# Kernel optimization log

Measured on AMD Instinct MI355X. Metric: run time of the kernel, lower is better.

The kernel has to match this reference:

```python
import jax, jax.numpy as jnp
import numpy as np

N_EMBD = 1024
N_HEAD = 16
BASE_SCALE = 0.03125  # config.base_scale
ATTN_ALPHA_INIT = 0.05
MLP_ALPHA_INIT = 0.05
SQK_INIT = 1.0
SUV_INIT = 1.0


def justnorm(x):
    return x / jnp.linalg.norm(x, axis=-1, keepdims=True)


def normalized_linear(x, W):
    # F.normalize(weight, p=2, dim=0): unit-norm columns of W [out, in] across the out dim
    Wn = W / jnp.linalg.norm(W, axis=0, keepdims=True)
    return x @ Wn.T


def setup_inputs() -> dict:
    key = jax.random.key(0)
    ks = jax.random.split(key, 8)
    C = N_EMBD
    s = 1.0 / np.sqrt(C)
    inp = {
        "h": jax.random.normal(ks[0], (8, 1024, C), dtype=jnp.float32),
        "Wq": jax.random.normal(ks[1], (C, C), dtype=jnp.float32) * s,
        "Wk": jax.random.normal(ks[2], (C, C), dtype=jnp.float32) * s,
        "Wv": jax.random.normal(ks[3], (C, C), dtype=jnp.float32) * s,
        "Wo": jax.random.normal(ks[4], (C, C), dtype=jnp.float32) * s,
        "Wfc": jax.random.normal(ks[5], (8 * C, C), dtype=jnp.float32) * s,
        "Wproj": jax.random.normal(ks[6], (C, 4 * C), dtype=jnp.float32) * (1.0 / np.sqrt(4 * C)),
        "sqk": jnp.full((C,), SQK_INIT * BASE_SCALE, dtype=jnp.float32),
        "suv": jnp.full((8 * C,), SUV_INIT * 1.0, dtype=jnp.float32),
        "attn_alpha": jnp.full((C,), BASE_SCALE, dtype=jnp.float32),
        "mlp_alpha": jnp.full((C,), BASE_SCALE, dtype=jnp.float32),
    }
    return inp


def reference(h, Wq, Wk, Wv, Wo, Wfc, Wproj, sqk, suv, attn_alpha, mlp_alpha):
    B, T, C = h.shape
    H, D = N_HEAD, C // N_HEAD

    # ---- attention ----
    q = normalized_linear(h, Wq).reshape(B, T, H, D).transpose(0, 2, 1, 3)  # bhtd
    k = normalized_linear(h, Wk).reshape(B, T, H, D).transpose(0, 2, 1, 3)
    v = normalized_linear(h, Wv).reshape(B, T, H, D).transpose(0, 2, 1, 3)

    sqk_s = (sqk * (SQK_INIT / BASE_SCALE)).reshape(1, H, 1, D)  # per-(head, head_dim) scale
    q = sqk_s * justnorm(q)
    k = sqk_s * justnorm(k)

    softmax_scale = float(D) ** 0.5  # nGPT uses sqrt(head_dim)
    att = jax.nn.softmax(jnp.einsum("bhqd,bhkd->bhqk", q, k) * softmax_scale, axis=-1)
    y = jnp.einsum("bhqk,bhkd->bhqd", att, v)
    y = y.transpose(0, 2, 1, 3).reshape(B, T, C)
    h_att = normalized_linear(y, Wo)

    lr = jnp.abs(attn_alpha * (ATTN_ALPHA_INIT / BASE_SCALE))
    A = justnorm(h)
    Bn = justnorm(h_att)
    h = justnorm(A + lr * (Bn - A))

    # ---- SwiGLU MLP ----
    uv = h @ Wfc.T  # [B,T,8C]
    suv_s = suv * (SUV_INIT / 1.0 * (C ** 0.5))
    uv = suv_s * uv
    u, vg = jnp.split(uv, 2, axis=-1)
    x_mlp = u * jax.nn.silu(vg)
    h_mlp = x_mlp @ Wproj.T

    lr = jnp.abs(mlp_alpha * (MLP_ALPHA_INIT / BASE_SCALE))
    A = justnorm(h)
    Bn = justnorm(h_mlp)
    h = justnorm(A + lr * (Bn - A))
    return h
```

## Files before the change

kernel.cpp:

```cpp
#include <hip/hip_runtime.h>

typedef __attribute__((ext_vector_type(8))) short s8v;
typedef __attribute__((ext_vector_type(4))) short s4v;
typedef __attribute__((ext_vector_type(4))) float f4v;

#define MFMA __builtin_amdgcn_mfma_f32_16x16x32_bf16

__device__ __forceinline__ float b2f(unsigned short b) {
  union { unsigned u; float f; } x; x.u = ((unsigned)b) << 16; return x.f;
}
__device__ __forceinline__ unsigned short f2b(float f) {
  union { float f; unsigned u; } x; x.f = f;
  unsigned r = x.u + 0x7fffu + ((x.u >> 16) & 1u);
  return (unsigned short)(r >> 16);
}
__device__ __forceinline__ void gl_lds16(const void* g, void* l) {
  __builtin_amdgcn_global_load_lds(
      (const __attribute__((address_space(1))) unsigned int*)g,
      (__attribute__((address_space(3))) unsigned int*)l, 16, 0, 0);
}

__global__ void colsq4(const float* __restrict__ Wq, const float* __restrict__ Wk,
                       const float* __restrict__ Wv, const float* __restrict__ Wo,
                       float* __restrict__ cs) {
  const int z = blockIdx.z;
  const float* W = (z == 0) ? Wq : (z == 1) ? Wk : (z == 2) ? Wv : Wo;
  int j = blockIdx.x * 256 + threadIdx.x;
  const float* p = W + (long)(blockIdx.y * 64) * 1024 + j;
  float s = 0.f;
#pragma unroll 4
  for (int n = 0; n < 64; ++n) { float v = p[(long)n * 1024]; s += v * v; }
  atomicAdd(&cs[z * 1024 + j], s);
}

__global__ void convw4(const float* __restrict__ Wq, const float* __restrict__ Wk,
                       const float* __restrict__ Wv, const float* __restrict__ Wo,
                       const float* __restrict__ cs, unsigned short* __restrict__ dst) {
  const int y = blockIdx.y;
  const float* src = (y == 0) ? Wq : (y == 1) ? Wk : (y == 2) ? Wv : Wo;
  long idx = ((long)blockIdx.x * 256 + threadIdx.x) << 2;
  float4 v = *(const float4*)(src + idx);
  const float* c = cs + y * 1024 + (int)(idx & 1023);
  s4v o;
  o[0] = (short)f2b(v.x * rsqrtf(c[0]));
  o[1] = (short)f2b(v.y * rsqrtf(c[1]));
  o[2] = (short)f2b(v.z * rsqrtf(c[2]));
  o[3] = (short)f2b(v.w * rsqrtf(c[3]));
  *(s4v*)(dst + (long)y * 1048576 + idx) = o;
}

__global__ void cast3(const float* __restrict__ Wfc, const float* __restrict__ Wpj,
                      const float* __restrict__ h, unsigned short* __restrict__ Wfc_b,
                      unsigned short* __restrict__ Wpj_b, unsigned short* __restrict__ h_b) {
  int bid = blockIdx.x;
  const float* src; unsigned short* dst;
  if (bid < 8192) { src = Wfc; dst = Wfc_b; }
  else if (bid < 12288) { src = Wpj; dst = Wpj_b; bid -= 8192; }
  else { src = h; dst = h_b; bid -= 12288; }
  long idx = ((long)bid * 256 + threadIdx.x) << 2;
  float4 v = *(const float4*)(src + idx);
  s4v o;
  o[0] = (short)f2b(v.x); o[1] = (short)f2b(v.y);
  o[2] = (short)f2b(v.z); o[3] = (short)f2b(v.w);
  *(s4v*)(dst + idx) = o;
}

__global__ __launch_bounds__(256) void gemm_bt(
    const unsigned short* __restrict__ A, const unsigned short* __restrict__ B,
    unsigned short* __restrict__ Cout, int K, int ldc) {
  __shared__ unsigned short smem[32768];
  const int tid = threadIdx.x, lane = tid & 63, w = tid >> 6;
  const int quad = lane >> 4, lq = lane & 15;
  const int wy = w >> 1, wx = w & 1;
  const int m0 = blockIdx.y << 7, n0 = blockIdx.x << 7;

  const int trow = tid >> 2;
  const int cb = ((tid & 3) ^ ((tid >> 3) & 3)) << 3;
  const unsigned short* Ag0 = A + (long)(m0 + trow) * K + cb;
  const unsigned short* Ag1 = A + (long)(m0 + 64 + trow) * K + cb;
  const unsigned short* Bg0 = B + (long)(n0 + trow) * K + cb;
  const unsigned short* Bg1 = B + (long)(n0 + 64 + trow) * K + cb;
  unsigned short* l0 = smem + (tid << 3);

  const int swz = ((lq >> 1) & 3) << 4;
  const int aoff = (wy * 64 + lq) * 64 + ((quad << 4) ^ swz);
  const int boff = 8192 + (wx * 64 + lq) * 64 + ((quad << 4) ^ swz);

  f4v acc[4][4];
  f4v zero = {0.f, 0.f, 0.f, 0.f};
#pragma unroll
  for (int i = 0; i < 4; ++i)
#pragma unroll
    for (int j = 0; j < 4; ++j) acc[i][j] = zero;

  auto stage = [&](int T) {
    const int bo = (T & 3) << 13;
    const int col = T << 5;
    gl_lds16(Ag0 + col, l0 + bo);
    gl_lds16(Ag1 + col, l0 + bo + 2048);
    gl_lds16(Bg0 + col, l0 + bo + 4096);
    gl_lds16(Bg1 + col, l0 + bo + 6144);
  };
  const char* sb = (const char*)smem;
  auto compute = [&](int kt) {
    const int bo = (kt & 3) << 14;
    s8v a[4], b[4];
#pragma unroll
    for (int i = 0; i < 4; ++i) a[i] = *(const s8v*)(sb + bo + aoff + i * 1024);
#pragma unroll
    for (int j = 0; j < 4; ++j) b[j] = *(const s8v*)(sb + bo + boff + j * 1024);
    __builtin_amdgcn_s_setprio(1);
#pragma unroll
    for (int i = 0; i < 4; ++i)
#pragma unroll
      for (int j = 0; j < 4; ++j)
        acc[i][j] = MFMA(a[i], b[j], acc[i][j], 0, 0, 0);
    __builtin_amdgcn_s_setprio(0);
  };

  const int nt = K >> 5;
  stage(0); stage(1); stage(2);
  for (int kt = 0; kt < nt - 2; ++kt) {
    asm volatile("s_waitcnt vmcnt(8)" ::: "memory");
    __builtin_amdgcn_s_barrier();
    asm volatile("" ::: "memory");
    if (kt < nt - 3) stage(kt + 3);
    compute(kt);
  }
  asm volatile("s_waitcnt vmcnt(4)" ::: "memory");
  __builtin_amdgcn_s_barrier();
  asm volatile("" ::: "memory");
  compute(nt - 2);
  asm volatile("s_waitcnt vmcnt(0)" ::: "memory");
  __builtin_amdgcn_s_barrier();
  asm volatile("" ::: "memory");
  compute(nt - 1);

  __syncthreads();
#pragma unroll
  for (int i = 0; i < 4; ++i)
#pragma unroll
    for (int j = 0; j < 4; ++j)
#pragma unroll
      for (int r = 0; r < 4; ++r) {
        int row = wy * 64 + i * 16 + quad * 4 + r;
        int col = wx * 64 + j * 16 + lq;
        smem[row * 136 + col] = f2b(acc[i][j][r]);
      }
  __syncthreads();
#pragma unroll
  for (int it = 0; it < 8; ++it) {
    int row = it * 16 + (tid >> 4);
    int col = (tid & 15) << 3;
    s8v v = *(const s8v*)(smem + row * 136 + col);
    *(s8v*)(Cout + (long)(m0 + row) * ldc + n0 + col) = v;
  }
}

__global__ __launch_bounds__(256) void gemm_qkv(
    const unsigned short* __restrict__ A, const unsigned short* __restrict__ B,
    unsigned short* __restrict__ Cout, unsigned short* __restrict__ Vt,
    const float* __restrict__ sqk) {
  __shared__ unsigned short smem[32768];
  const int tid = threadIdx.x, lane = tid & 63, w = tid >> 6;
  const int quad = lane >> 4, lq = lane & 15;
  const int wy = w >> 1, wx = w & 1;
  const int m0 = blockIdx.y << 7, n0 = blockIdx.x << 7;
  const int K = 1024;

  const int trow = tid >> 2;
  const int cb = ((tid & 3) ^ ((tid >> 3) & 3)) << 3;
  const unsigned short* Ag0 = A + (long)(m0 + trow) * K + cb;
  const unsigned short* Ag1 = A + (long)(m0 + 64 + trow) * K + cb;
  const unsigned short* Bg0 = B + (long)(n0 + trow) * K + cb;
  const unsigned short* Bg1 = B + (long)(n0 + 64 + trow) * K + cb;
  unsigned short* l0 = smem + (tid << 3);

  const int swz = ((lq >> 1) & 3) << 4;
  const int aoff = (wy * 64 + lq) * 64 + ((quad << 4) ^ swz);
  const int boff = 8192 + (wx * 64 + lq) * 64 + ((quad << 4) ^ swz);

  f4v acc[4][4];
  f4v zero = {0.f, 0.f, 0.f, 0.f};
#pragma unroll
  for (int i = 0; i < 4; ++i)
#pragma unroll
    for (int j = 0; j < 4; ++j) acc[i][j] = zero;

  auto stage = [&](int T) {
    const int bo = (T & 3) << 13;
    const int col = T << 5;
    gl_lds16(Ag0 + col, l0 + bo);
    gl_lds16(Ag1 + col, l0 + bo + 2048);
    gl_lds16(Bg0 + col, l0 + bo + 4096);
    gl_lds16(Bg1 + col, l0 + bo + 6144);
  };
  const char* sb = (const char*)smem;
  auto compute = [&](int kt) {
    const int bo = (kt & 3) << 14;
    s8v a[4], b[4];
#pragma unroll
    for (int i = 0; i < 4; ++i) a[i] = *(const s8v*)(sb + bo + aoff + i * 1024);
#pragma unroll
    for (int j = 0; j < 4; ++j) b[j] = *(const s8v*)(sb + bo + boff + j * 1024);
    __builtin_amdgcn_s_setprio(1);
#pragma unroll
    for (int i = 0; i < 4; ++i)
#pragma unroll
      for (int j = 0; j < 4; ++j)
        acc[i][j] = MFMA(a[i], b[j], acc[i][j], 0, 0, 0);
    __builtin_amdgcn_s_setprio(0);
  };

  stage(0); stage(1); stage(2);
  for (int kt = 0; kt < 30; ++kt) {
    asm volatile("s_waitcnt vmcnt(8)" ::: "memory");
    __builtin_amdgcn_s_barrier();
    asm volatile("" ::: "memory");
    if (kt < 29) stage(kt + 3);
    compute(kt);
  }
  asm volatile("s_waitcnt vmcnt(4)" ::: "memory");
  __builtin_amdgcn_s_barrier();
  asm volatile("" ::: "memory");
  compute(30);
  asm volatile("s_waitcnt vmcnt(0)" ::: "memory");
  __builtin_amdgcn_s_barrier();
  asm volatile("" ::: "memory");
  compute(31);

  if (n0 < 2048) {
    float sc[4];
#pragma unroll
    for (int j = 0; j < 4; ++j)
      sc[j] = sqk[(n0 + wx * 64 + j * 16 + lq) & 1023] * 32.f;
#pragma unroll
    for (int i = 0; i < 4; ++i)
#pragma unroll
      for (int r = 0; r < 4; ++r) {
        float ss = 0.f;
#pragma unroll
        for (int j = 0; j < 4; ++j) ss += acc[i][j][r] * acc[i][j][r];
        ss += __shfl_xor(ss, 1, 64); ss += __shfl_xor(ss, 2, 64);
        ss += __shfl_xor(ss, 4, 64); ss += __shfl_xor(ss, 8, 64);
        float rn = rsqrtf(ss);
#pragma unroll
        for (int j = 0; j < 4; ++j) acc[i][j][r] *= rn * sc[j];
      }
    __syncthreads();
#pragma unroll
    for (int i = 0; i < 4; ++i)
#pragma unroll
      for (int j = 0; j < 4; ++j)
#pragma unroll
        for (int r = 0; r < 4; ++r) {
          int row = wy * 64 + i * 16 + quad * 4 + r;
          int col = wx * 64 + j * 16 + lq;
          smem[row * 136 + col] = f2b(acc[i][j][r]);
        }
    __syncthreads();
#pragma unroll
    for (int it = 0; it < 8; ++it) {
      int row = it * 16 + (tid >> 4);
      int col = (tid & 15) << 3;
      s8v v = *(const s8v*)(smem + row * 136 + col);
      *(s8v*)(Cout + (long)(m0 + row) * 3072 + n0 + col) = v;
    }
  } else {
    __syncthreads();
#pragma unroll
    for (int i = 0; i < 4; ++i)
#pragma unroll
      for (int j = 0; j < 4; ++j) {
        int col = wx * 64 + j * 16 + lq;
        int rowb = wy * 64 + i * 16 + quad * 4;
        s4v pk;
#pragma unroll
        for (int r = 0; r < 4; ++r) pk[r] = (short)f2b(acc[i][j][r]);
        *(s4v*)(smem + col * 136 + rowb) = pk;
      }
    __syncthreads();
    {
      const int c = tid >> 1, half = tid & 1;
      const int f = (n0 - 2048) + c;
      const int bh = ((m0 >> 10) << 4) + (f >> 6);
      const int d = f & 63;
      unsigned short* dst = Vt + (long)(bh * 64 + d) * 1024 + (m0 & 1023) + half * 64;
      const unsigned short* src = smem + c * 136 + half * 64;
#pragma unroll
      for (int s = 0; s < 8; ++s)
        *(s8v*)(dst + s * 8) = *(const s8v*)(src + s * 8);
    }
  }
}

__global__ __launch_bounds__(512, 2) void gemm_fc(
    const unsigned short* __restrict__ A, const unsigned short* __restrict__ B,
    unsigned short* __restrict__ X, const float* __restrict__ suv) {
  __shared__ unsigned short smem[65536];
  const int tid = threadIdx.x, lane = tid & 63, w = tid >> 6;
  const int quad = lane >> 4, lq = lane & 15;
  const int wy = w >> 2, wx = w & 3;
  const int bid = blockIdx.x;
  const int xr = bid & 7, xq = bid >> 3;
  const int m0 = ((xr << 2) | (xq & 3)) << 8;
  const int n0 = (xq >> 2) << 7;

  const int trow = tid >> 3;
  const int scol = ((tid & 7) ^ (trow & 7)) << 3;
  const unsigned short* pA = A + (long)(m0 + trow) * 1024 + scol;
  const unsigned short* pB = B + (long)(n0 + trow) * 1024 + scol;
  unsigned short* ldst = smem + tid * 8;

  auto stA = [&](int tile, int half) {
    const int base = (tile & 1) * 32768 + half * 8192;
    const unsigned short* src = pA + (long)half * 131072 + (tile << 6);
    gl_lds16(src, ldst + base);
    gl_lds16(src + 65536, ldst + base + 4096);
  };
  auto stB = [&](int tile, int vh) {
    const int base = (tile & 1) * 32768 + 16384 + vh * 8192;
    const unsigned short* src = pB + (long)vh * 4194304 + (tile << 6);
    gl_lds16(src, ldst + base);
    gl_lds16(src + 65536, ldst + base + 4096);
  };

  const int rsw = (lq & 7) << 4;
  const int c0 = (quad * 16) ^ rsw;
  const int c1 = (64 + quad * 16) ^ rsw;
  const int aro = wy * 16384 + lq * 128;
  const int uro = 32768 + (wx * 32 + lq) * 128;
  const int vro = 49152 + (wx * 32 + lq) * 128;
  const char* sb = (const char*)smem;

  f4v aU[8][2], aV[8][2];
  f4v zero = {0.f, 0.f, 0.f, 0.f};
#pragma unroll
  for (int m = 0; m < 8; ++m)
#pragma unroll
    for (int j = 0; j < 2; ++j) { aU[m][j] = zero; aV[m][j] = zero; }

  s8v av[4][2], uf[2][2], vg[2][2];

  auto tile_phases = [&](int t, int bufB) {
#pragma unroll
    for (int m = 0; m < 4; ++m) {
      av[m][0] = *(const s8v*)(sb + bufB + aro + m * 2048 + c0);
      av[m][1] = *(const s8v*)(sb + bufB + aro + m * 2048 + c1);
    }
#pragma unroll
    for (int j = 0; j < 2; ++j) {
      uf[j][0] = *(const s8v*)(sb + bufB + uro + j * 2048 + c0);
      uf[j][1] = *(const s8v*)(sb + bufB + uro + j * 2048 + c1);
    }
    if (t < 15) stA(t + 1, 1);
    __builtin_amdgcn_s_barrier();
    asm volatile("" ::: "memory");
    __builtin_amdgcn_s_setprio(1);
#pragma unroll
    for (int m = 0; m < 4; ++m)
#pragma unroll
      for (int j = 0; j < 2; ++j) {
        aU[m][j] = MFMA(av[m][0], uf[j][0], aU[m][j], 0, 0, 0);
        aU[m][j] = MFMA(av[m][1], uf[j][1], aU[m][j], 0, 0, 0);
      }
    __builtin_amdgcn_s_setprio(0);
    asm volatile("" ::: "memory");
    __builtin_amdgcn_s_barrier();
    asm volatile("" ::: "memory");
#pragma unroll
    for (int j = 0; j < 2; ++j) {
      vg[j][0] = *(const s8v*)(sb + bufB + vro + j * 2048 + c0);
      vg[j][1] = *(const s8v*)(sb + bufB + vro + j * 2048 + c1);
    }
    if (t < 14) stB(t + 2, 0);
    __builtin_amdgcn_s_barrier();
    asm volatile("" ::: "memory");
    __builtin_amdgcn_s_setprio(1);
#pragma unroll
    for (int m = 0; m < 4; ++m)
#pragma unroll
      for (int j = 0; j < 2; ++j) {
        aV[m][j] = MFMA(av[m][0], vg[j][0], aV[m][j], 0, 0, 0);
        aV[m][j] = MFMA(av[m][1], vg[j][1], aV[m][j], 0, 0, 0);
      }
    __builtin_amdgcn_s_setprio(0);
    asm volatile("" ::: "memory");
    __builtin_amdgcn_s_barrier();
    asm volatile("" ::: "memory");
#pragma unroll
    for (int m = 0; m < 4; ++m) {
      av[m][0] = *(const s8v*)(sb + bufB + aro + (m + 4) * 2048 + c0);
      av[m][1] = *(const s8v*)(sb + bufB + aro + (m + 4) * 2048 + c1);
    }
    if (t < 14) stB(t + 2, 1);
    __builtin_amdgcn_s_barrier();
    asm volatile("" ::: "memory");
    __builtin_amdgcn_s_setprio(1);
#pragma unroll
    for (int m = 0; m < 4; ++m)
#pragma unroll
      for (int j = 0; j < 2; ++j) {
        aU[m + 4][j] = MFMA(av[m][0], uf[j][0], aU[m + 4][j], 0, 0, 0);
        aU[m + 4][j] = MFMA(av[m][1], uf[j][1], aU[m + 4][j], 0, 0, 0);
      }
    __builtin_amdgcn_s_setprio(0);
    asm volatile("" ::: "memory");
    __builtin_amdgcn_s_barrier();
    asm volatile("" ::: "memory");
    if (t < 14) stA(t + 2, 0);
    __builtin_amdgcn_s_barrier();
    asm volatile("" ::: "memory");
    __builtin_amdgcn_s_setprio(1);
#pragma unroll
    for (int m = 0; m < 4; ++m)
#pragma unroll
      for (int j = 0; j < 2; ++j) {
        aV[m + 4][j] = MFMA(av[m][0], vg[j][0], aV[m + 4][j], 0, 0, 0);
        aV[m + 4][j] = MFMA(av[m][1], vg[j][1], aV[m + 4][j], 0, 0, 0);
      }
    __builtin_amdgcn_s_setprio(0);
    if (t < 14) { asm volatile("s_waitcnt vmcnt(6)" ::: "memory"); }
    else if (t == 14) { asm volatile("s_waitcnt vmcnt(0)" ::: "memory"); }
    asm volatile("" ::: "memory");
    __builtin_amdgcn_s_barrier();
    asm volatile("" ::: "memory");
  };

  stB(0, 0); stB(0, 1); stA(0, 0); stA(0, 1);
  stB(1, 0); stB(1, 1); stA(1, 0);
  asm volatile("s_waitcnt vmcnt(6)" ::: "memory");
  __builtin_amdgcn_s_barrier();
  asm volatile("" ::: "memory");

  for (int tt = 0; tt < 8; ++tt) {
    tile_phases(tt * 2, 0);
    tile_phases(tt * 2 + 1, 65536);
  }

  float su[2], sv[2];
#pragma unroll
  for (int j = 0; j < 2; ++j) {
    su[j] = suv[n0 + wx * 32 + j * 16 + lq] * 32.f;
    sv[j] = suv[4096 + n0 + wx * 32 + j * 16 + lq] * 32.f;
  }
  __syncthreads();
#pragma unroll
  for (int m = 0; m < 8; ++m)
#pragma unroll
    for (int j = 0; j < 2; ++j)
#pragma unroll
      for (int r = 0; r < 4; ++r) {
        int row = wy * 128 + m * 16 + quad * 4 + r;
        int col = wx * 32 + j * 16 + lq;
        float uu = aU[m][j][r] * su[j];
        float vv = aV[m][j][r] * sv[j];
        float sig = 1.f / (1.f + __builtin_amdgcn_exp2f(vv * -1.44269504f));
        smem[row * 132 + col] = f2b(uu * vv * sig);
      }
  __syncthreads();
  {
    const int row = tid >> 1, half = tid & 1;
    unsigned short* dst = X + (long)(m0 + row) * 4096 + n0 + half * 64;
    const unsigned short* srcr = smem + row * 132 + half * 64;
#pragma unroll
    for (int s = 0; s < 8; ++s)
      *(s8v*)(dst + s * 8) = *(const s8v*)(srcr + s * 8);
  }
}

__global__ __launch_bounds__(256) void attn(const unsigned short* __restrict__ qkv,
                                            const unsigned short* __restrict__ Vt,
                                            unsigned short* __restrict__ Y) {
  __shared__ unsigned short smem[33792];
  unsigned short* Klds = smem;
  unsigned short* Vlds = smem + 8192;
  unsigned short* Plds = smem + 16384;
  const int tid = threadIdx.x, lane = tid & 63, w = tid >> 6;
  const int quad = lane >> 4, lq = lane & 15;
  const int bh = blockIdx.x, b = bh >> 4, h = bh & 15;
  const int qt = blockIdx.y;
  const int e0 = tid << 3;
  const int c_lo = e0 >> 10, row_s = (e0 & 1023) >> 3;
  const int vc_lo = e0 >> 9, vd = (e0 & 511) >> 3;

  s8v qf[2][2];
#pragma unroll
  for (int i = 0; i < 2; ++i)
#pragma unroll
    for (int ks = 0; ks < 2; ++ks) {
      int row = qt * 128 + w * 32 + i * 16 + lq;
      qf[i][ks] = *(const s8v*)(qkv + (long)(b * 1024 + row) * 3072 + h * 64 + ks * 32 + quad * 8);
    }

  f4v o[2][4];
  float lp[2][4];
  f4v zero = {0.f, 0.f, 0.f, 0.f};
#pragma unroll
  for (int i = 0; i < 2; ++i) {
#pragma unroll
    for (int nf = 0; nf < 4; ++nf) o[i][nf] = zero;
#pragma unroll
    for (int r = 0; r < 4; ++r) lp[i][r] = 0.f;
  }

  const unsigned short* Kg = qkv + (long)(b * 1024 + row_s) * 3072 + 1024 + h * 64 + (c_lo << 3);
  const unsigned short* Vg = Vt + (long)(bh * 64 + vd) * 1024 + (vc_lo << 3);
  unsigned short* Pw = Plds + w * 4352;

  for (int kt0 = 0; kt0 < 1024; kt0 += 128) {
    __syncthreads();
#pragma unroll
    for (int it = 0; it < 4; ++it) {
      gl_lds16(Kg + (long)kt0 * 3072 + it * 16, Klds + it * 2048 + e0);
      gl_lds16(Vg + kt0 + it * 32, Vlds + it * 2048 + e0);
    }
    __syncthreads();
    f4v s[2][8];
#pragma unroll
    for (int i = 0; i < 2; ++i)
#pragma unroll
      for (int j = 0; j < 8; ++j) s[i][j] = zero;
#pragma unroll
    for (int ks = 0; ks < 2; ++ks)
#pragma unroll
      for (int j = 0; j < 8; ++j) {
        s8v kf = *(const s8v*)(Klds + (ks * 4 + quad) * 1024 + (j * 16 + lq) * 8);
        s[0][j] = MFMA(qf[0][ks], kf, s[0][j], 0, 0, 0);
        s[1][j] = MFMA(qf[1][ks], kf, s[1][j], 0, 0, 0);
      }
#pragma unroll
    for (int i = 0; i < 2; ++i)
#pragma unroll
      for (int j = 0; j < 8; ++j)
#pragma unroll
        for (int r = 0; r < 4; ++r) {
          float p = __builtin_amdgcn_exp2f(s[i][j][r] * 11.5415603f - 11.5415603f);
          lp[i][r] += p;
          Pw[(i * 16 + quad * 4 + r) * 136 + j * 16 + lq] = f2b(p);
        }
    s8v pf[2][4];
#pragma unroll
    for (int i = 0; i < 2; ++i)
#pragma unroll
      for (int ks = 0; ks < 4; ++ks)
        pf[i][ks] = *(const s8v*)(Pw + (i * 16 + lq) * 136 + ks * 32 + quad * 8);
#pragma unroll
    for (int nf = 0; nf < 4; ++nf)
#pragma unroll
      for (int ks = 0; ks < 4; ++ks) {
        s8v vf = *(const s8v*)(Vlds + (ks * 4 + quad) * 512 + (nf * 16 + lq) * 8);
        o[0][nf] = MFMA(pf[0][ks], vf, o[0][nf], 0, 0, 0);
        o[1][nf] = MFMA(pf[1][ks], vf, o[1][nf], 0, 0, 0);
      }
  }
#pragma unroll
  for (int i = 0; i < 2; ++i)
#pragma unroll
    for (int r = 0; r < 4; ++r) {
      float v = lp[i][r];
      v += __shfl_xor(v, 1, 64); v += __shfl_xor(v, 2, 64);
      v += __shfl_xor(v, 4, 64); v += __shfl_xor(v, 8, 64);
      lp[i][r] = 1.f / v;
    }
#pragma unroll
  for (int i = 0; i < 2; ++i)
#pragma unroll
    for (int nf = 0; nf < 4; ++nf)
#pragma unroll
      for (int r = 0; r < 4; ++r) {
        int row = qt * 128 + w * 32 + i * 16 + quad * 4 + r;
        Y[(long)(b * 1024 + row) * 1024 + h * 64 + nf * 16 + lq] = f2b(o[i][nf][r] * lp[i][r]);
      }
}

__global__ __launch_bounds__(256) void residual(
    const float* __restrict__ hin, const unsigned short* __restrict__ hbr,
    const float* __restrict__ alpha, float* __restrict__ outf,
    unsigned short* __restrict__ outb) {
  __shared__ float red[8];
  const int tid = threadIdx.x, lane = tid & 63, w = tid >> 6;
  const long base = (long)blockIdx.x * 1024;
  float hv[4], bvv[4];
  float s1 = 0.f, s2 = 0.f;
#pragma unroll
  for (int k = 0; k < 4; ++k) {
    int c = k * 256 + tid;
    hv[k] = hin[base + c];
    bvv[k] = b2f(hbr[base + c]);
    s1 += hv[k] * hv[k]; s2 += bvv[k] * bvv[k];
  }
#pragma unroll
  for (int m = 1; m < 64; m <<= 1) { s1 += __shfl_xor(s1, m, 64); s2 += __shfl_xor(s2, m, 64); }
  if (lane == 0) { red[w] = s1; red[4 + w] = s2; }
  __syncthreads();
  s1 = red[0] + red[1] + red[2] + red[3];
  s2 = red[4] + red[5] + red[6] + red[7];
  float rn1 = rsqrtf(s1), rn2 = rsqrtf(s2);
  float z[4], s3 = 0.f;
#pragma unroll
  for (int k = 0; k < 4; ++k) {
    int c = k * 256 + tid;
    float a = hv[k] * rn1;
    float lr = fabsf(alpha[c]) * 1.6f;
    float zz = a + lr * (bvv[k] * rn2 - a);
    z[k] = zz; s3 += zz * zz;
  }
#pragma unroll
  for (int m = 1; m < 64; m <<= 1) s3 += __shfl_xor(s3, m, 64);
  __syncthreads();
  if (lane == 0) red[w] = s3;
  __syncthreads();
  s3 = red[0] + red[1] + red[2] + red[3];
  float rn3 = rsqrtf(s3);
#pragma unroll
  for (int k = 0; k < 4; ++k) {
    int c = k * 256 + tid;
    float ov = z[k] * rn3;
    if (outf) outf[base + c] = ov;
    if (outb) outb[base + c] = f2b(ov);
  }
}

extern "C" void kernel_launch(void* const* d_in, const int* in_sizes, int n_in,
                              void* d_out, int out_size, void* d_ws, size_t ws_size,
                              hipStream_t stream) {
  const float* h   = (const float*)d_in[0];
  const float* Wq  = (const float*)d_in[1];
  const float* Wk  = (const float*)d_in[2];
  const float* Wv  = (const float*)d_in[3];
  const float* Wo  = (const float*)d_in[4];
  const float* Wfc = (const float*)d_in[5];
  const float* Wpj = (const float*)d_in[6];
  const float* sqk = (const float*)d_in[7];
  const float* suv = (const float*)d_in[8];
  const float* aat = (const float*)d_in[9];
  const float* aml = (const float*)d_in[10];
  float* out = (float*)d_out;

  char* ws = (char*)d_ws;
  size_t off = 0;
  auto alloc = [&](size_t n) { char* p = ws + off; off += (n + 255) & ~(size_t)255; return p; };
  float* cs4   = (float*)alloc(16384);
  unsigned short* Wqkv_b = (unsigned short*)alloc(3ull * 1024 * 1024 * 2);
  unsigned short* Wo_b   = (unsigned short*)alloc(1024ull * 1024 * 2);
  unsigned short* Wfc_b  = (unsigned short*)alloc(8192ull * 1024 * 2);
  unsigned short* Wpj_b  = (unsigned short*)alloc(1024ull * 4096 * 2);
  unsigned short* slotC  = (unsigned short*)alloc(8192ull * 1024 * 2);
  unsigned short* slotD  = (unsigned short*)alloc(8192ull * 4096 * 2);
  unsigned short* slotE  = (unsigned short*)alloc(8192ull * 1024 * 2);
  unsigned short* y_b    = (unsigned short*)alloc(8192ull * 1024 * 2);
  float*          h2_f   = (float*)alloc(8192ull * 1024 * 4);

  unsigned short* h_b    = slotC;
  unsigned short* hmlp_b = slotC;
  unsigned short* qkv_r  = slotD;
  unsigned short* xmlp   = slotD;
  unsigned short* hatt_b = slotD + 25165824;
  unsigned short* Vt     = slotE;
  unsigned short* h2_b   = slotE;

  hipMemsetAsync(ws, 0, 16384, stream);
  colsq4<<<dim3(4, 16, 4), 256, 0, stream>>>(Wq, Wk, Wv, Wo, cs4);
  convw4<<<dim3(1024, 4), 256, 0, stream>>>(Wq, Wk, Wv, Wo, cs4, Wqkv_b);
  cast3<<<20480, 256, 0, stream>>>(Wfc, Wpj, h, Wfc_b, Wpj_b, h_b);
  gemm_qkv<<<dim3(24, 64), 256, 0, stream>>>(h_b, Wqkv_b, qkv_r, Vt, sqk);
  attn<<<dim3(128, 8), 256, 0, stream>>>(qkv_r, Vt, y_b);
  gemm_bt<<<dim3(8, 64), 256, 0, stream>>>(y_b, Wo_b, hatt_b, 1024, 1024);
  residual<<<8192, 256, 0, stream>>>(h, hatt_b, aat, h2_f, h2_b);
  gemm_fc<<<1024, 512, 0, stream>>>(h2_b, Wfc_b, xmlp, suv);
  gemm_bt<<<dim3(8, 64), 256, 0, stream>>>(xmlp, Wpj_b, hmlp_b, 4096, 1024);
  residual<<<8192, 256, 0, stream>>>(h2_f, hmlp_b, aml, out, nullptr);
}
```

Baseline: 592.2 us.

## Replace 128x128 output GEMM with 256x128 eight-wave tile and interleaved staging

The generic gemm_bt kernel used for the attention output projection and the MLP down projection is replaced by gemm_pj. It uses a 256x128 tile with 512 threads, a K-step of 64 and double buffering, and interleaves its global-to-LDS stages between the MFMA phases. The larger tile raises data reuse per block and spreads load issue across the compute phases. The cost is 256 blocks on a 256-CU-class device, which can leave few waves per CU and tail effects, plus more LDS per block.

```diff
diff --git a/kernel.cpp b/kernel.cpp
--- a/kernel.cpp
+++ b/kernel.cpp
@@ -65,95 +65,149 @@
   *(s4v*)(dst + idx) = o;
 }
 
-__global__ __launch_bounds__(256) void gemm_bt(
+__global__ __launch_bounds__(512, 1) void gemm_pj(
     const unsigned short* __restrict__ A, const unsigned short* __restrict__ B,
-    unsigned short* __restrict__ Cout, int K, int ldc) {
-  __shared__ unsigned short smem[32768];
+    unsigned short* __restrict__ Cout, int K) {
+  __shared__ unsigned short smem[49152];
   const int tid = threadIdx.x, lane = tid & 63, w = tid >> 6;
   const int quad = lane >> 4, lq = lane & 15;
-  const int wy = w >> 1, wx = w & 1;
-  const int m0 = blockIdx.y << 7, n0 = blockIdx.x << 7;
-
-  const int trow = tid >> 2;
-  const int cb = ((tid & 3) ^ ((tid >> 3) & 3)) << 3;
-  const unsigned short* Ag0 = A + (long)(m0 + trow) * K + cb;
-  const unsigned short* Ag1 = A + (long)(m0 + 64 + trow) * K + cb;
-  const unsigned short* Bg0 = B + (long)(n0 + trow) * K + cb;
-  const unsigned short* Bg1 = B + (long)(n0 + 64 + trow) * K + cb;
-  unsigned short* l0 = smem + (tid << 3);
-
-  const int swz = ((lq >> 1) & 3) << 4;
-  const int aoff = (wy * 64 + lq) * 64 + ((quad << 4) ^ swz);
-  const int boff = 8192 + (wx * 64 + lq) * 64 + ((quad << 4) ^ swz);
-
-  f4v acc[4][4];
+  const int wy = w >> 2, wx = w & 3;
+  const int bid = blockIdx.x;
+  const int m0 = (bid >> 3) << 8, n0 = (bid & 7) << 7;
+
+  const int trow = tid >> 3;
+  const int scol = ((tid & 7) ^ (trow & 7)) << 3;
+  const unsigned short* pA = A + (long)(m0 + trow) * K + scol;
+  const unsigned short* pB = B + (long)(n0 + trow) * K + scol;
+  unsigned short* ldst = smem + tid * 8;
+  const long a64 = (long)64 * K;
+
+  auto stA = [&](int t, int half) {
+    const int base = (t & 1) * 24576 + half * 8192;
+    const unsigned short* src = pA + (long)half * 128 * K + (t << 6);
+    gl_lds16(src, ldst + base);
+    gl_lds16(src + a64, ldst + base + 4096);
+  };
+  auto stB = [&](int t) {
+    const int base = (t & 1) * 24576 + 16384;
+    const unsigned short* src = pB + (t << 6);
+    gl_lds16(src, ldst + base);
+    gl_lds16(src + a64, ldst + base + 4096);
+  };
+
+  const int rsw = (lq & 7) << 4;
+  const int c0 = (quad * 16) ^ rsw;
+  const int c1 = (64 + quad * 16) ^ rsw;
+  const int aro = wy * 16384 + lq * 128;
+  const int bro = 32768 + (wx * 32 + lq) * 128;
+  const char* sb = (const char*)smem;
+
+  f4v acc[8][2];
   f4v zero = {0.f, 0.f, 0.f, 0.f};
 #pragma unroll
-  for (int i = 0; i < 4; ++i)
-#pragma unroll
-    for (int j = 0; j < 4; ++j) acc[i][j] = zero;
-
-  auto stage = [&](int T) {
-    const int bo = (T & 3) << 13;
-    const int col = T << 5;
-    gl_lds16(Ag0 + col, l0 + bo);
-    gl_lds16(Ag1 + col, l0 + bo + 2048);
-    gl_lds16(Bg0 + col, l0 + bo + 4096);
-    gl_lds16(Bg1 + col, l0 + bo + 6144);
-  };
-  const char* sb = (const char*)smem;
-  auto compute = [&](int kt) {
-    const int bo = (kt & 3) << 14;
-    s8v a[4], b[4];
-#pragma unroll
-    for (int i = 0; i < 4; ++i) a[i] = *(const s8v*)(sb + bo + aoff + i * 1024);
-#pragma unroll
-    for (int j = 0; j < 4; ++j) b[j] = *(const s8v*)(sb + bo + boff + j * 1024);
-    __builtin_amdgcn_s_setprio(1);
-#pragma unroll
-    for (int i = 0; i < 4; ++i)
-#pragma unroll
-      for (int j = 0; j < 4; ++j)
-        acc[i][j] = MFMA(a[i], b[j], acc[i][j], 0, 0, 0);
-    __builtin_amdgcn_s_setprio(0);
-  };
-
-  const int nt = K >> 5;
-  stage(0); stage(1); stage(2);
-  for (int kt = 0; kt < nt - 2; ++kt) {
-    asm volatile("s_waitcnt vmcnt(8)" ::: "memory");
-    __builtin_amdgcn_s_barrier();
-    asm volatile("" ::: "memory");
-    if (kt < nt - 3) stage(kt + 3);
-    compute(kt);
-  }
+  for (int m = 0; m < 8; ++m)
+#pragma unroll
+    for (int j = 0; j < 2; ++j) acc[m][j] = zero;
+
+  s8v av[4][2], bf[2][2];
+
+  stB(0); stA(0, 0); stA(0, 1); stB(1); stA(1, 0);
   asm volatile("s_waitcnt vmcnt(4)" ::: "memory");
   __builtin_amdgcn_s_barrier();
   asm volatile("" ::: "memory");
-  compute(nt - 2);
-  asm volatile("s_waitcnt vmcnt(0)" ::: "memory");
-  __builtin_amdgcn_s_barrier();
-  asm volatile("" ::: "memory");
-  compute(nt - 1);
+
+  const int nt = K >> 6;
+  for (int t = 0; t < nt; ++t) {
+    const int bo = (t & 1) * 49152;
+#pragma unroll
+    for (int m = 0; m < 4; ++m) {
+      av[m][0] = *(const s8v*)(sb + bo + aro + m * 2048 + c0);
+      av[m][1] = *(const s8v*)(sb + bo + aro + m * 2048 + c1);
+    }
+#pragma unroll
+    for (int j = 0; j < 2; ++j) {
+      bf[j][0] = *(const s8v*)(sb + bo + bro + j * 2048 + c0);
+      bf[j][1] = *(const s8v*)(sb + bo + bro + j * 2048 + c1);
+    }
+    if (t < nt - 1) stA(t + 1, 1);
+    __builtin_amdgcn_s_barrier();
+    asm volatile("" ::: "memory");
+    __builtin_amdgcn_s_setprio(1);
+#pragma unroll
+    for (int m = 0; m < 4; ++m)
+#pragma unroll
+      for (int j = 0; j < 2; ++j)
+        acc[m][j] = MFMA(av[m][0], bf[j][0], acc[m][j], 0, 0, 0);
+    __builtin_amdgcn_s_setprio(0);
+    asm volatile("" ::: "memory");
+    __builtin_amdgcn_s_barrier();
+    asm volatile("" ::: "memory");
+    if (t < nt - 2) stB(t + 2);
+    __builtin_amdgcn_s_barrier();
+    asm volatile("" ::: "memory");
+    __builtin_amdgcn_s_setprio(1);
+#pragma unroll
+    for (int m = 0; m < 4; ++m)
+#pragma unroll
+      for (int j = 0; j < 2; ++j)
+        acc[m][j] = MFMA(av[m][1], bf[j][1], acc[m][j], 0, 0, 0);
+    __builtin_amdgcn_s_setprio(0);
+    asm volatile("" ::: "memory");
+    __builtin_amdgcn_s_barrier();
+    asm volatile("" ::: "memory");
+#pragma unroll
+    for (int m = 0; m < 4; ++m) {
+      av[m][0] = *(const s8v*)(sb + bo + aro + (m + 4) * 2048 + c0);
+      av[m][1] = *(const s8v*)(sb + bo + aro + (m + 4) * 2048 + c1);
+    }
+    __builtin_amdgcn_s_barrier();
+    asm volatile("" ::: "memory");
+    __builtin_amdgcn_s_setprio(1);
+#pragma unroll
+    for (int m = 0; m < 4; ++m)
+#pragma unroll
+      for (int j = 0; j < 2; ++j)
+        acc[m + 4][j] = MFMA(av[m][0], bf[j][0], acc[m + 4][j], 0, 0, 0);
+    __builtin_amdgcn_s_setprio(0);
+    asm volatile("" ::: "memory");
+    __builtin_amdgcn_s_barrier();
+    asm volatile("" ::: "memory");
+    if (t < nt - 2) stA(t + 2, 0);
+    __builtin_amdgcn_s_barrier();
+    asm volatile("" ::: "memory");
+    __builtin_amdgcn_s_setprio(1);
+#pragma unroll
+    for (int m = 0; m < 4; ++m)
+#pragma unroll
+      for (int j = 0; j < 2; ++j)
+        acc[m + 4][j] = MFMA(av[m][1], bf[j][1], acc[m + 4][j], 0, 0, 0);
+    __builtin_amdgcn_s_setprio(0);
+    if (t < nt - 2) { asm volatile("s_waitcnt vmcnt(4)" ::: "memory"); }
+    else if (t == nt - 2) { asm volatile("s_waitcnt vmcnt(0)" ::: "memory"); }
+    asm volatile("" ::: "memory");
+    __builtin_amdgcn_s_barrier();
+    asm volatile("" ::: "memory");
+  }
 
   __syncthreads();
 #pragma unroll
-  for (int i = 0; i < 4; ++i)
-#pragma unroll
-    for (int j = 0; j < 4; ++j)
+  for (int m = 0; m < 8; ++m)
+#pragma unroll
+    for (int j = 0; j < 2; ++j)
 #pragma unroll
       for (int r = 0; r < 4; ++r) {
-        int row = wy * 64 + i * 16 + quad * 4 + r;
-        int col = wx * 64 + j * 16 + lq;
-        smem[row * 136 + col] = f2b(acc[i][j][r]);
+        int row = wy * 128 + m * 16 + quad * 4 + r;
+        int col = wx * 32 + j * 16 + lq;
+        smem[row * 132 + col] = f2b(acc[m][j][r]);
       }
   __syncthreads();
-#pragma unroll
-  for (int it = 0; it < 8; ++it) {
-    int row = it * 16 + (tid >> 4);
-    int col = (tid & 15) << 3;
-    s8v v = *(const s8v*)(smem + row * 136 + col);
-    *(s8v*)(Cout + (long)(m0 + row) * ldc + n0 + col) = v;
+  {
+    const int row = tid >> 1, half = tid & 1;
+    unsigned short* dst = Cout + (long)(m0 + row) * 1024 + n0 + half * 64;
+    const unsigned short* src = smem + row * 132 + half * 64;
+#pragma unroll
+    for (int s = 0; s < 8; ++s)
+      *(s8v*)(dst + s * 8) = *(const s8v*)(src + s * 8);
   }
 }
 
@@ -666,9 +720,9 @@
   cast3<<<20480, 256, 0, stream>>>(Wfc, Wpj, h, Wfc_b, Wpj_b, h_b);
   gemm_qkv<<<dim3(24, 64), 256, 0, stream>>>(h_b, Wqkv_b, qkv_r, Vt, sqk);
   attn<<<dim3(128, 8), 256, 0, stream>>>(qkv_r, Vt, y_b);
-  gemm_bt<<<dim3(8, 64), 256, 0, stream>>>(y_b, Wo_b, hatt_b, 1024, 1024);
+  gemm_pj<<<256, 512, 0, stream>>>(y_b, Wo_b, hatt_b, 1024);
   residual<<<8192, 256, 0, stream>>>(h, hatt_b, aat, h2_f, h2_b);
   gemm_fc<<<1024, 512, 0, stream>>>(h2_b, Wfc_b, xmlp, suv);
-  gemm_bt<<<dim3(8, 64), 256, 0, stream>>>(xmlp, Wpj_b, hmlp_b, 4096, 1024);
+  gemm_pj<<<256, 512, 0, stream>>>(xmlp, Wpj_b, hmlp_b, 4096);
   residual<<<8192, 256, 0, stream>>>(h2_f, hmlp_b, aml, out, nullptr);
 }
```

Result: no change. 597.0 us (+0.8%).
